# Optimization experiments

Measured on AMD Instinct MI355X. Metric: run time of the kernel, lower is better.

## Reference

```python
import jax, jax.numpy as jnp
import numpy as np

jax.config.update("jax_enable_x64", True)

MANT_SCALE = 8388608.0  # 2**23


def _decode_fp32_bits(bits):
    """[..., 32] {0,1} pulses (MSB-first IEEE-754 float32) -> float64 value."""
    f64 = jnp.float64
    sign = 1.0 - 2.0 * bits[..., 0].astype(f64)
    e = jnp.einsum('...j,j->...', bits[..., 1:9].astype(f64),
                   jnp.exp2(jnp.arange(7, -1, -1, dtype=f64)))
    frac = jnp.einsum('...j,j->...', bits[..., 9:32].astype(f64),
                      jnp.exp2(-jnp.arange(1, 24, dtype=f64)))
    normal = sign * jnp.exp2(e - 127.0) * (1.0 + frac)
    subnorm = sign * jnp.exp2(-126.0) * frac
    return jnp.where(e > 0, normal, subnorm)


def _encode_fp32_bits(y):
    """float64 value already on the fp32 grid -> [..., 32] {0,1} pulses (MSB-first)."""
    f64 = jnp.float64
    sbit = (y < 0).astype(f64)
    a = jnp.abs(y)
    e = jnp.clip(jnp.floor(jnp.log2(jnp.where(a > 0, a, 1.0))), -126.0, 127.0)
    eb = jnp.where(a > 0, e + 127.0, 0.0)          # biased exponent, 0 for zero/subnormal
    frac = jnp.where(eb > 0, a * jnp.exp2(-e) - 1.0, a * jnp.exp2(126.0))
    mant = frac * MANT_SCALE                        # exact integer for fp32-grid y
    ebits = jnp.mod(jnp.floor(eb[..., None] * jnp.exp2(-jnp.arange(7, -1, -1, dtype=f64))), 2.0)
    mbits = jnp.mod(jnp.floor(mant[..., None] * jnp.exp2(-jnp.arange(22, -1, -1, dtype=f64))), 2.0)
    bits = jnp.concatenate([sbit[..., None], ebits, mbits], axis=-1)
    return jnp.where((a > 0)[..., None], bits, 0.0).astype(jnp.float32)


def setup_inputs() -> dict:
    rng = np.random.default_rng(0)
    vals = (rng.standard_normal((1, 2048, 1024)) * 2.0).astype(np.float32)
    words = vals.view(np.uint32)
    shifts = np.arange(31, -1, -1, dtype=np.uint32)
    bits = ((words[..., None] >> shifts) & np.uint32(1)).astype(np.float32)
    return {"x": jnp.asarray(bits)}


def reference(x):
    # GELU(x) ~= x * sigmoid(1.702 * x), all intermediates in fp64 (as the
    # gate-level pipeline does), final result rounded once to fp32 bits.
    xv = _decode_fp32_bits(x)
    y64 = xv * jax.nn.sigmoid(1.702 * xv)
    y32 = y64.astype(jnp.float32).astype(jnp.float64)  # FP64 -> FP32 rounding
    return _encode_fp32_bits(y32)
```

## Files before the change

### kernel.cpp

```cpp
#include <hip/hip_runtime.h>
#include <math.h>


#define LN2C 0x1.62e42fefa39efp-1

__global__ __launch_bounds__(256) void build_tables(double* __restrict__ dt,
                                                    uint32_t* __restrict__ et) {
#pragma clang fp contract(off)
  const double LN2 = LN2C;
  __shared__ double Wdec[8], Lms[23];
  const int t = threadIdx.x;
  if (t < 8) Wdec[t] = exp((double)(7 - t) * LN2);
  if (t >= 31 && t < 54) Lms[t - 31] = exp((double)(31 - t) * LN2);
  __syncthreads();

  if (t == 0) {
    dt[0] = exp(-126.0 * LN2);
    et[0] = 0u;
  } else {
    double e_c = 0.0;
#pragma unroll
    for (int j = 0; j < 8; ++j)
      if ((t >> (7 - j)) & 1) e_c = e_c + Wdec[j];
    dt[t] = exp((e_c - 127.0) * LN2);
  }
  if (t < 23) dt[256 + t] = exp((double)(-1 - t) * LN2);
  if (t < 23) dt[279 + t] = Lms[t];
  if (t < 254) {
    double e0 = (double)(t - 126);
    dt[302 + t] = exp(-e0 * LN2);
  }
  if (t >= 1 && t < 255) {
    double eb = (double)t;
    uint32_t r = 0;
#pragma unroll
    for (int sc = 7; sc >= 0; --sc) {
      double f = floor(eb * Lms[sc]);
      double md = f - 2.0 * floor(0.5 * f);
      r |= ((uint32_t)md) << (23 + sc);
    }
    et[t] = r;
  }
}

__global__ __launch_bounds__(256) void spike_gelu_kernel(
    const uint4* __restrict__ in, uint4* __restrict__ out,
    const double* __restrict__ dt, const uint32_t* __restrict__ et,
    int n_vals) {
#pragma clang fp contract(off)
  const double LN2 = LN2C;
  __shared__ double dtab[556];
  __shared__ uint32_t etab[256];
  __shared__ uint32_t lds_w[256];

  const int tid = threadIdx.x;
  for (int i = tid; i < 556; i += 256) dtab[i] = dt[i];
  if (tid < 255) etab[tid] = et[tid];

  const int n_chunks = n_vals * 8;
  const int blk_chunk0 = blockIdx.x * 2048;

  const int nibshift = 28 - 4 * (tid & 7);
#pragma unroll
  for (int i = 0; i < 8; ++i) {
    int g = blk_chunk0 + i * 256 + tid;
    uint32_t nib = 0;
    if (g < n_chunks) {
      uint4 b = in[g];
      nib = (((b.x >> 23) & 1u) << 3) | (((b.y >> 23) & 1u) << 2) |
            (((b.z >> 23) & 1u) << 1) | ((b.w >> 23) & 1u);
    }
    uint32_t part = nib << nibshift;
    part |= __shfl_xor(part, 1);
    part |= __shfl_xor(part, 2);
    part |= __shfl_xor(part, 4);
    if ((tid & 7) == 0) lds_w[i * 32 + (tid >> 3)] = part;
  }
  __syncthreads();

  const int v = blockIdx.x * 256 + tid;
  uint32_t ob = 0;
  if (v < n_vals) {
    const uint32_t w = lds_w[tid];
    const double* E1t  = dtab;
    const double* Vdec = dtab + 256;
    const double* Lm   = dtab + 279;
    const double* P2t  = dtab + 302;

    double sign = (w >> 31) ? -1.0 : 1.0;
    double frac_d = 0.0;
#pragma unroll
    for (int j = 0; j < 23; ++j)
      if ((w >> (22 - j)) & 1u) frac_d = frac_d + Vdec[j];

    const uint32_t eidx = (w >> 23) & 0xFFu;
    double x;
    if (eidx > 0) x = (sign * E1t[eidx]) * (1.0 + frac_d);
    else          x = (sign * E1t[0]) * frac_d;

    double t = 1.702 * x;
    double s = 1.0 / (1.0 + exp(-t));
    double y = x * s;
    float yf = (float)y;
    double yd = (double)yf;

    double a = fabs(yd);
    if (a > 0.0) {
      if (yd < 0.0) ob |= 0x80000000u;
      uint32_t yb = __float_as_uint(yf);
      uint32_t Ef = (yb >> 23) & 0xFFu;
      uint32_t mb = yb & 0x7FFFFFu;
      int e0i;
      if (Ef == 0u) {
        e0i = -126;
      } else if (mb != 0u) {
        e0i = (int)Ef - 127;
      } else {
        double e0 = floor(log(a) / LN2);
        e0 = fmin(fmax(e0, -126.0), 127.0);
        e0i = (int)e0;
      }
      double p2 = P2t[e0i + 126];
      double m1 = a * p2;
      double frac_e = m1 - 1.0;
      double mant = frac_e * 8388608.0;
      ob |= etab[e0i + 127];
#pragma unroll
      for (int sc = 22; sc >= 0; --sc) {
        double f = floor(mant * Lm[sc]);
        ob |= (uint32_t)(((int)f) & 1) << sc;
      }
    }
  }
  lds_w[tid] = ob;
  __syncthreads();

#pragma unroll
  for (int i = 0; i < 8; ++i) {
    int g = blk_chunk0 + i * 256 + tid;
    if (g < n_chunks) {
      uint32_t wv = lds_w[i * 32 + (tid >> 3)];
      int base = 31 - 4 * (tid & 7);
      uint4 o;
      o.x = ((wv >> base) & 1u) * 0x3F800000u;
      o.y = ((wv >> (base - 1)) & 1u) * 0x3F800000u;
      o.z = ((wv >> (base - 2)) & 1u) * 0x3F800000u;
      o.w = ((wv >> (base - 3)) & 1u) * 0x3F800000u;
      out[g] = o;
    }
  }
}

extern "C" void kernel_launch(void* const* d_in, const int* in_sizes, int n_in,
                              void* d_out, int out_size, void* d_ws, size_t ws_size,
                              hipStream_t stream) {
  int n_vals = in_sizes[0] / 32;
  double* dt = (double*)d_ws;
  uint32_t* et = (uint32_t*)((char*)d_ws + 556 * sizeof(double));
  build_tables<<<1, 256, 0, stream>>>(dt, et);
  const int block = 256;
  int grid = (n_vals + block - 1) / block;
  spike_gelu_kernel<<<grid, block, 0, stream>>>(
      (const uint4*)d_in[0], (uint4*)d_out, dt, et, n_vals);
}
```

Measured before the change: 432.0 us.

## Process two values per thread with nontemporal I/O and a shorter mantissa encode loop

Each thread now handles two fp32 values, so each block covers 512 values and the grid is halved. Global loads and stores become nontemporal vector accesses. The mantissa encode no longer runs the 23-step floor loop for every bit: it takes the integer mantissa from rint and only reruns the floor check on the low bits up to the trailing-zero count. The log-based exponent path is kept only for exact powers of two, as a rarely taken branch. This targets memory-bound streaming and the per-bit double-precision work, but it raises register pressure and leans on an integer shortcut for mantissa bits that has to match the floor-based reference exactly.

```diff
diff --git a/kernel.cpp b/kernel.cpp
--- a/kernel.cpp
+++ b/kernel.cpp
@@ -3,6 +3,8 @@
 
 
 #define LN2C 0x1.62e42fefa39efp-1
+
+typedef unsigned int u32x4 __attribute__((ext_vector_type(4)));
 
 __global__ __launch_bounds__(256) void build_tables(double* __restrict__ dt,
                                                     uint32_t* __restrict__ et) {
@@ -44,109 +46,147 @@
 }
 
 __global__ __launch_bounds__(256) void spike_gelu_kernel(
-    const uint4* __restrict__ in, uint4* __restrict__ out,
+    const u32x4* __restrict__ in, u32x4* __restrict__ out,
     const double* __restrict__ dt, const uint32_t* __restrict__ et,
     int n_vals) {
 #pragma clang fp contract(off)
   const double LN2 = LN2C;
   __shared__ double dtab[556];
   __shared__ uint32_t etab[256];
-  __shared__ uint32_t lds_w[256];
+  __shared__ uint32_t lds_w[512];
 
   const int tid = threadIdx.x;
   for (int i = tid; i < 556; i += 256) dtab[i] = dt[i];
-  if (tid < 255) etab[tid] = et[tid];
+  etab[tid] = et[tid];
 
   const int n_chunks = n_vals * 8;
-  const int blk_chunk0 = blockIdx.x * 2048;
+  const int blk_chunk0 = blockIdx.x * 4096;
 
   const int nibshift = 28 - 4 * (tid & 7);
 #pragma unroll
   for (int i = 0; i < 8; ++i) {
-    int g = blk_chunk0 + i * 256 + tid;
-    uint32_t nib = 0;
-    if (g < n_chunks) {
-      uint4 b = in[g];
-      nib = (((b.x >> 23) & 1u) << 3) | (((b.y >> 23) & 1u) << 2) |
-            (((b.z >> 23) & 1u) << 1) | ((b.w >> 23) & 1u);
-    }
-    uint32_t part = nib << nibshift;
-    part |= __shfl_xor(part, 1);
-    part |= __shfl_xor(part, 2);
-    part |= __shfl_xor(part, 4);
-    if ((tid & 7) == 0) lds_w[i * 32 + (tid >> 3)] = part;
+    int g0 = blk_chunk0 + i * 256 + tid;
+    int g1 = g0 + 2048;
+    uint32_t nib0 = 0, nib1 = 0;
+    if (g0 < n_chunks) {
+      u32x4 b = __builtin_nontemporal_load(&in[g0]);
+      nib0 = (((b.x >> 23) & 1u) << 3) | (((b.y >> 23) & 1u) << 2) |
+             (((b.z >> 23) & 1u) << 1) | ((b.w >> 23) & 1u);
+    }
+    if (g1 < n_chunks) {
+      u32x4 b = __builtin_nontemporal_load(&in[g1]);
+      nib1 = (((b.x >> 23) & 1u) << 3) | (((b.y >> 23) & 1u) << 2) |
+             (((b.z >> 23) & 1u) << 1) | ((b.w >> 23) & 1u);
+    }
+    uint32_t p0 = nib0 << nibshift, p1 = nib1 << nibshift;
+    p0 |= __shfl_xor(p0, 1);  p1 |= __shfl_xor(p1, 1);
+    p0 |= __shfl_xor(p0, 2);  p1 |= __shfl_xor(p1, 2);
+    p0 |= __shfl_xor(p0, 4);  p1 |= __shfl_xor(p1, 4);
+    if ((tid & 7) == 0) {
+      lds_w[i * 32 + (tid >> 3)] = p0;
+      lds_w[256 + i * 32 + (tid >> 3)] = p1;
+    }
   }
   __syncthreads();
 
-  const int v = blockIdx.x * 256 + tid;
-  uint32_t ob = 0;
-  if (v < n_vals) {
-    const uint32_t w = lds_w[tid];
-    const double* E1t  = dtab;
-    const double* Vdec = dtab + 256;
-    const double* Lm   = dtab + 279;
-    const double* P2t  = dtab + 302;
-
-    double sign = (w >> 31) ? -1.0 : 1.0;
-    double frac_d = 0.0;
-#pragma unroll
-    for (int j = 0; j < 23; ++j)
-      if ((w >> (22 - j)) & 1u) frac_d = frac_d + Vdec[j];
-
-    const uint32_t eidx = (w >> 23) & 0xFFu;
-    double x;
-    if (eidx > 0) x = (sign * E1t[eidx]) * (1.0 + frac_d);
-    else          x = (sign * E1t[0]) * frac_d;
-
-    double t = 1.702 * x;
-    double s = 1.0 / (1.0 + exp(-t));
-    double y = x * s;
-    float yf = (float)y;
-    double yd = (double)yf;
-
-    double a = fabs(yd);
-    if (a > 0.0) {
-      if (yd < 0.0) ob |= 0x80000000u;
-      uint32_t yb = __float_as_uint(yf);
-      uint32_t Ef = (yb >> 23) & 0xFFu;
-      uint32_t mb = yb & 0x7FFFFFu;
-      int e0i;
-      if (Ef == 0u) {
-        e0i = -126;
-      } else if (mb != 0u) {
-        e0i = (int)Ef - 127;
-      } else {
-        double e0 = floor(log(a) / LN2);
-        e0 = fmin(fmax(e0, -126.0), 127.0);
-        e0i = (int)e0;
-      }
-      double p2 = P2t[e0i + 126];
-      double m1 = a * p2;
-      double frac_e = m1 - 1.0;
-      double mant = frac_e * 8388608.0;
-      ob |= etab[e0i + 127];
-#pragma unroll
-      for (int sc = 22; sc >= 0; --sc) {
-        double f = floor(mant * Lm[sc]);
-        ob |= (uint32_t)(((int)f) & 1) << sc;
-      }
-    }
-  }
-  lds_w[tid] = ob;
+  const int v0 = blockIdx.x * 512 + tid;
+  const int v1 = v0 + 256;
+  const bool ok0 = v0 < n_vals, ok1 = v1 < n_vals;
+  const uint32_t w0 = lds_w[tid], w1 = lds_w[256 + tid];
+  const double* E1t  = dtab;
+  const double* Vdec = dtab + 256;
+  const double* Lm   = dtab + 279;
+  const double* P2t  = dtab + 302;
+
+  double f0 = 0.0, f1 = 0.0;
+#pragma unroll
+  for (int j = 0; j < 23; ++j) {
+    double vj = Vdec[j];
+    if ((w0 >> (22 - j)) & 1u) f0 = f0 + vj;
+    if ((w1 >> (22 - j)) & 1u) f1 = f1 + vj;
+  }
+  uint32_t ei0 = (w0 >> 23) & 0xFFu, ei1 = (w1 >> 23) & 0xFFu;
+  double sg0 = (w0 >> 31) ? -1.0 : 1.0, sg1 = (w1 >> 31) ? -1.0 : 1.0;
+  double fa0 = ei0 ? (1.0 + f0) : f0, fa1 = ei1 ? (1.0 + f1) : f1;
+  double x0 = (sg0 * E1t[ei0]) * fa0, x1 = (sg1 * E1t[ei1]) * fa1;
+
+  double t0 = 1.702 * x0, t1 = 1.702 * x1;
+  double e0v = exp(-t0), e1v = exp(-t1);
+  double s0 = 1.0 / (1.0 + e0v), s1 = 1.0 / (1.0 + e1v);
+  double y0 = x0 * s0, y1 = x1 * s1;
+  float yf0 = (float)y0, yf1 = (float)y1;
+  double yd0 = (double)yf0, yd1 = (double)yf1;
+
+  double a0 = fabs(yd0), a1 = fabs(yd1);
+  uint32_t yb0 = __float_as_uint(yf0), yb1 = __float_as_uint(yf1);
+  uint32_t Ef0 = (yb0 >> 23) & 0xFFu, Ef1 = (yb1 >> 23) & 0xFFu;
+  uint32_t mbf0 = yb0 & 0x7FFFFFu, mbf1 = yb1 & 0x7FFFFFu;
+  int e00 = (Ef0 == 0u) ? -126 : (int)Ef0 - 127;
+  int e01 = (Ef1 == 0u) ? -126 : (int)Ef1 - 127;
+  bool pw0 = ok0 && (a0 > 0.0) && (Ef0 != 0u) && (mbf0 == 0u);
+  bool pw1 = ok1 && (a1 > 0.0) && (Ef1 != 0u) && (mbf1 == 0u);
+  if (__builtin_expect(pw0 || pw1, 0)) {
+    if (pw0) {
+      double e0 = floor(log(a0) / LN2);
+      e00 = (int)fmin(fmax(e0, -126.0), 127.0);
+    }
+    if (pw1) {
+      double e0 = floor(log(a1) / LN2);
+      e01 = (int)fmin(fmax(e0, -126.0), 127.0);
+    }
+  }
+  double p20 = P2t[e00 + 126], p21 = P2t[e01 + 126];
+  double m10 = a0 * p20, m11 = a1 * p21;
+  double mant0 = (m10 - 1.0) * 8388608.0;
+  double mant1 = (m11 - 1.0) * 8388608.0;
+  int M0 = (int)rint(mant0), M1 = (int)rint(mant1);
+  uint32_t mb0 = ((uint32_t)M0) & 0x7FFFFFu, mb1 = ((uint32_t)M1) & 0x7FFFFFu;
+  int T0 = M0 ? __builtin_ctz((uint32_t)M0) : 23;
+  int T1 = M1 ? __builtin_ctz((uint32_t)M1) : 23;
+  int L0 = T0 < 22 ? T0 : 22, L1 = T1 < 22 ? T1 : 22;
+  int Lmax = L0 > L1 ? L0 : L1;
+  for (int sc = 0; sc <= Lmax; ++sc) {
+    double lm = Lm[sc];
+    if (sc <= L0) {
+      double f = floor(mant0 * lm);
+      mb0 = (mb0 & ~(1u << sc)) | (((uint32_t)(((int)f) & 1)) << sc);
+    }
+    if (sc <= L1) {
+      double f = floor(mant1 * lm);
+      mb1 = (mb1 & ~(1u << sc)) | (((uint32_t)(((int)f) & 1)) << sc);
+    }
+  }
+  uint32_t ob0 = (yb0 & 0x80000000u) | etab[e00 + 127] | mb0;
+  uint32_t ob1 = (yb1 & 0x80000000u) | etab[e01 + 127] | mb1;
+  ob0 = (ok0 && a0 > 0.0) ? ob0 : 0u;
+  ob1 = (ok1 && a1 > 0.0) ? ob1 : 0u;
+
+  lds_w[tid] = ob0;
+  lds_w[256 + tid] = ob1;
   __syncthreads();
 
 #pragma unroll
   for (int i = 0; i < 8; ++i) {
-    int g = blk_chunk0 + i * 256 + tid;
-    if (g < n_chunks) {
-      uint32_t wv = lds_w[i * 32 + (tid >> 3)];
-      int base = 31 - 4 * (tid & 7);
-      uint4 o;
-      o.x = ((wv >> base) & 1u) * 0x3F800000u;
-      o.y = ((wv >> (base - 1)) & 1u) * 0x3F800000u;
-      o.z = ((wv >> (base - 2)) & 1u) * 0x3F800000u;
-      o.w = ((wv >> (base - 3)) & 1u) * 0x3F800000u;
-      out[g] = o;
+    int g0 = blk_chunk0 + i * 256 + tid;
+    int g1 = g0 + 2048;
+    int base = 31 - 4 * (tid & 7);
+    uint32_t wv0 = lds_w[i * 32 + (tid >> 3)];
+    uint32_t wv1 = lds_w[256 + i * 32 + (tid >> 3)];
+    if (g0 < n_chunks) {
+      u32x4 o;
+      o.x = ((wv0 >> base) & 1u) * 0x3F800000u;
+      o.y = ((wv0 >> (base - 1)) & 1u) * 0x3F800000u;
+      o.z = ((wv0 >> (base - 2)) & 1u) * 0x3F800000u;
+      o.w = ((wv0 >> (base - 3)) & 1u) * 0x3F800000u;
+      __builtin_nontemporal_store(o, &out[g0]);
+    }
+    if (g1 < n_chunks) {
+      u32x4 o;
+      o.x = ((wv1 >> base) & 1u) * 0x3F800000u;
+      o.y = ((wv1 >> (base - 1)) & 1u) * 0x3F800000u;
+      o.z = ((wv1 >> (base - 2)) & 1u) * 0x3F800000u;
+      o.w = ((wv1 >> (base - 3)) & 1u) * 0x3F800000u;
+      __builtin_nontemporal_store(o, &out[g1]);
     }
   }
 }
@@ -158,8 +198,7 @@
   double* dt = (double*)d_ws;
   uint32_t* et = (uint32_t*)((char*)d_ws + 556 * sizeof(double));
   build_tables<<<1, 256, 0, stream>>>(dt, et);
-  const int block = 256;
-  int grid = (n_vals + block - 1) / block;
-  spike_gelu_kernel<<<grid, block, 0, stream>>>(
-      (const uint4*)d_in[0], (uint4*)d_out, dt, et, n_vals);
+  int grid = (n_vals + 511) / 512;
+  spike_gelu_kernel<<<grid, 256, 0, stream>>>(
+      (const u32x4*)d_in[0], (u32x4*)d_out, dt, et, n_vals);
 }
```

Measured after the change: 426.2 us. Within noise of the previous version (-1.3%).
